# Performance work log

Measured on AMD Instinct MI355X. Metric: run time of the kernel, lower is better.

The kernel has to match this reference:

```python
import jax, jax.numpy as jnp
import numpy as np

# ---- config (matches init_kwargs) ----
C_IN, C_OUT = 128, 128
HYPER_OUT = 64            # hyper_out_size in DoubleConv
KB = C_IN // HYPER_OUT    # k = 2 blocks along input channels
HB = C_OUT // HYPER_OUT   # h = 2 blocks along output channels
Z_DIM, HID, SEIDEL_DIM = 128, 128, 48
R, F = 8, 3               # num_radii, filter size
BN_EPS = 1e-5


def _mlp_bank(z, W1, b1, W2, b2):
    # z: (S,); W1: (M,S,HID); returns (M, HID) embeddings from M distinct MLPs
    h = jax.nn.relu(jnp.einsum('s,msh->mh', z, W1) + b1)
    return jax.nn.relu(jnp.einsum('mh,mhg->mg', h, W2) + b2)


def _hyper(e, hw2, hb2, hw1, hb1):
    # Ha-style hypernetwork: e (Z_DIM,) -> kernel (64, 64, R, F, F)
    h_in = (e @ hw2 + hb2).reshape(HYPER_OUT, Z_DIM)
    h_fin = h_in @ hw1 + hb1  # (64, 64*R*F*F)
    return h_fin.reshape(HYPER_OUT, HYPER_OUT, R, F, F)


def _assemble(kernels, rows, cols):
    # kernels: (rows*cols, 64, 64, R, F, F) -> (rows*64, cols*64, R, F, F)
    k = kernels.reshape(rows, cols, HYPER_OUT, HYPER_OUT, R, F, F)
    k = k.transpose(0, 2, 1, 3, 4, 5, 6)
    return k.reshape(rows * HYPER_OUT, cols * HYPER_OUT, R, F, F)


def _interp_radii(w, Wdim):
    # trilinear interpolate (R,F,F)->(Wdim,F,F); F->F is identity, so linear along R
    # align_corners=False (PyTorch default)
    src = (jnp.arange(Wdim, dtype=jnp.float32) + 0.5) * (R / Wdim) - 0.5
    src = jnp.clip(src, 0.0, R - 1.0)
    i0 = jnp.floor(src).astype(jnp.int32)
    i1 = jnp.minimum(i0 + 1, R - 1)
    t = (src - i0.astype(jnp.float32))[None, None, :, None, None]
    return w[:, :, i0] * (1.0 - t) + w[:, :, i1] * t  # (co, ci, Wdim, F, F)


def _lri_conv(x, w):
    # x: (c_in, H, W); w: (c_out, c_in, R, F, F); padding=1, k=3
    c_in, H, W = x.shape
    xp = jnp.concatenate([x[:, -1:, :], x, x[:, :1, :]], axis=1)  # circular pad H
    xp = jnp.pad(xp, ((0, 0), (0, 0), (1, 1)))                    # zero pad W
    # patches laid out (c, di, dj) to match F.unfold
    pat = jnp.stack([xp[:, di:di + H, dj:dj + W]
                     for di in range(3) for dj in range(3)], axis=1)  # (c_in, 9, H, W)
    pat = pat.reshape(c_in * 9, H, W).transpose(1, 2, 0)              # (H, W, c_in*9)
    wi = _interp_radii(w, W)                                          # (co, ci, W, F, F)
    wu = wi.transpose(0, 2, 1, 3, 4).reshape(w.shape[0], W, c_in * 9) # (co, W, ci*9)
    return jnp.einsum('hwj,cwj->chw', pat, wu)                        # (co, H, W)


def _bn_eval(x, gamma, beta):
    # eval-mode BatchNorm2d with running_mean=0, running_var=1
    scale = gamma / jnp.sqrt(1.0 + BN_EPS)
    return x * scale[:, None, None] + beta[:, None, None]


def setup_inputs() -> dict:
    key = jax.random.key(0)
    ks = jax.random.split(key, 20)
    B, H, W = 2, 256, 128
    n1 = HB * KB   # 4 MLPs for first conv
    n2 = HB * HB   # 4 MLPs for second conv
    inp = {
        'x': jax.random.normal(ks[0], (B, C_IN, H, W), jnp.float32),
        'seidel': jax.random.normal(ks[1], (B, SEIDEL_DIM), jnp.float32),
        'm1_W1': jax.random.normal(ks[2], (n1, SEIDEL_DIM, HID)) * 0.1,
        'm1_b1': jnp.zeros((n1, HID)),
        'm1_W2': jax.random.normal(ks[3], (n1, HID, HID)) * 0.08,
        'm1_b2': jnp.zeros((n1, HID)),
        'm2_W1': jax.random.normal(ks[4], (n2, SEIDEL_DIM, HID)) * 0.1,
        'm2_b1': jnp.zeros((n2, HID)),
        'm2_W2': jax.random.normal(ks[5], (n2, HID, HID)) * 0.08,
        'm2_b2': jnp.zeros((n2, HID)),
        'hyp_w2': jax.random.normal(ks[6], (Z_DIM, HYPER_OUT * Z_DIM)) * 0.02,
        'hyp_b2': jnp.zeros((HYPER_OUT * Z_DIM,)),
        'hyp_w1': jax.random.normal(ks[7], (Z_DIM, HYPER_OUT * R * F * F)) * 0.02,
        'hyp_b1': jnp.zeros((HYPER_OUT * R * F * F,)),
        'bn1_g': jnp.ones((C_OUT,)), 'bn1_b': jnp.zeros((C_OUT,)),
        'bn2_g': jnp.ones((C_OUT,)), 'bn2_b': jnp.zeros((C_OUT,)),
    }
    return inp


def reference(x, seidel, m1_W1, m1_b1, m1_W2, m1_b2, m2_W1, m2_b1, m2_W2, m2_b2,
              hyp_w2, hyp_b2, hyp_w1, hyp_b1, bn1_g, bn1_b, bn2_g, bn2_b):
    hyper = lambda e: _hyper(e, hyp_w2, hyp_b2, hyp_w1, hyp_b1)

    def one_sample(x_i, z_i):
        emb1 = _mlp_bank(z_i, m1_W1, m1_b1, m1_W2, m1_b2)   # (h*k, Z)
        w1 = _assemble(jax.vmap(hyper)(emb1), HB, KB)        # (c_out, c_in, R, F, F)
        emb2 = _mlp_bank(z_i, m2_W1, m2_b1, m2_W2, m2_b2)   # (h*h, Z)
        w2 = _assemble(jax.vmap(hyper)(emb2), HB, HB)        # (c_out, c_out, R, F, F)
        y = jax.nn.relu(_bn_eval(_lri_conv(x_i, w1), bn1_g, bn1_b))
        y = jax.nn.relu(_bn_eval(_lri_conv(y, w2), bn2_g, bn2_b))
        return y

    return jax.vmap(one_sample)(x, seidel)  # (B, c_out, H, W)
```

## Files before the change

### kernel.cpp

```cpp
#include <hip/hip_runtime.h>
#include <hip/hip_bf16.h>

typedef _Float16 f16;
typedef _Float16 half8 __attribute__((ext_vector_type(8)));
typedef _Float16 half4_t __attribute__((ext_vector_type(4)));
typedef float floatx16 __attribute__((ext_vector_type(16)));

__device__ __forceinline__ void gll16(const void* g, void* l) {
    __builtin_amdgcn_global_load_lds(
        (const __attribute__((address_space(1))) void*)g,
        (__attribute__((address_space(3))) void*)l, 16, 0, 0);
}

__global__ __launch_bounds__(256) void embed_a(
    const float* __restrict__ seidel,
    const float* __restrict__ m1W1, const float* __restrict__ m1b1,
    const float* __restrict__ m1W2, const float* __restrict__ m1b2,
    const float* __restrict__ m2W1, const float* __restrict__ m2b1,
    const float* __restrict__ m2W2, const float* __restrict__ m2b2,
    float* __restrict__ eout)
{
    int combo = blockIdx.x;
    int s = combo >> 3, conv = (combo >> 2) & 1, m = combo & 3;
    const float* W1 = conv ? m2W1 : m1W1;
    const float* b1 = conv ? m2b1 : m1b1;
    const float* W2 = conv ? m2W2 : m1W2;
    const float* b2 = conv ? m2b2 : m1b2;
    __shared__ float zs[48], hbuf[128];
    int tid = threadIdx.x;
    if (tid < 48) zs[tid] = seidel[s*48 + tid];
    __syncthreads();
    if (tid < 128) {
        float a = b1[m*128 + tid];
        for (int i = 0; i < 48; ++i) a += zs[i] * W1[(m*48 + i)*128 + tid];
        hbuf[tid] = fmaxf(a, 0.f);
    }
    __syncthreads();
    if (tid < 128) {
        float a = b2[m*128 + tid];
        for (int i = 0; i < 128; ++i) a += hbuf[i] * W2[(m*128 + i)*128 + tid];
        eout[combo*128 + tid] = fmaxf(a, 0.f);
    }
}

__global__ __launch_bounds__(128) void embed_b3(
    const float* __restrict__ eout, const float* __restrict__ hw2,
    const float* __restrict__ hb2, float* __restrict__ hin)
{
    __shared__ float es[16][128];
    int tid = threadIdx.x;
    int j = blockIdx.x*128 + tid;
    for (int i = tid; i < 2048; i += 128) es[i >> 7][i & 127] = eout[i];
    __syncthreads();
    float acc[16];
    float b = hb2[j];
    #pragma unroll
    for (int c = 0; c < 16; ++c) acc[c] = b;
    for (int i = 0; i < 128; ++i) {
        float wv = hw2[(size_t)i*8192 + j];
        #pragma unroll
        for (int c = 0; c < 16; ++c) acc[c] += es[c][i]*wv;
    }
    #pragma unroll
    for (int c = 0; c < 16; ++c) hin[(size_t)c*8192 + j] = acc[c];
}

__global__ void hw1t_kernel(const float* __restrict__ in, float* __restrict__ out)
{
    __shared__ float tile[32][33];
    int j0 = blockIdx.x*32, k0 = blockIdx.y*32;
    int tx = threadIdx.x, ty = threadIdx.y;
    #pragma unroll
    for (int i = 0; i < 4; ++i) tile[ty + i*8][tx] = in[(size_t)(k0 + ty + i*8)*4608 + j0 + tx];
    __syncthreads();
    #pragma unroll
    for (int i = 0; i < 4; ++i) out[(size_t)(j0 + ty + i*8)*128 + k0 + tx] = tile[tx][ty + i*8];
}

__global__ __launch_bounds__(256) void hfin2_kernel(
    const float* __restrict__ hin, const float* __restrict__ hw1t,
    const float* __restrict__ hb1, f16* __restrict__ wtab)
{
    int c72 = blockIdx.x;
    int combo = blockIdx.y;
    int r = c72 / 9, tap = c72 - r*9;
    int s = combo >> 3, conv = (combo >> 2) & 1, m = combo & 3;
    __shared__ float hl[64][132];
    __shared__ float wt[64][132];
    __shared__ f16 ct[64][72];
    int tid = threadIdx.x;
    const float4* hsrc = (const float4*)(hin + (size_t)combo*8192);
    for (int i = tid; i < 2048; i += 256) {
        int a = i >> 5, kq = i & 31;
        *(float4*)&hl[a][kq*4] = hsrc[i];
    }
    for (int i = tid; i < 2048; i += 256) {
        int b = i >> 5, kq = i & 31;
        *(float4*)&wt[b][kq*4] = *(const float4*)(hw1t + (size_t)(b*72 + c72)*128 + kq*4);
    }
    __syncthreads();
    int ta = tid >> 4, tb = tid & 15;
    int a0 = ta*4, b0 = tb*4;
    float acc[4][4] = {};
    #pragma unroll 4
    for (int k4 = 0; k4 < 32; ++k4) {
        float4 A[4], B[4];
        #pragma unroll
        for (int i = 0; i < 4; ++i) A[i] = *(const float4*)&hl[a0 + i][k4*4];
        #pragma unroll
        for (int i = 0; i < 4; ++i) B[i] = *(const float4*)&wt[b0 + i][k4*4];
        #pragma unroll
        for (int i = 0; i < 4; ++i)
            #pragma unroll
            for (int j2 = 0; j2 < 4; ++j2)
                acc[i][j2] += A[i].x*B[j2].x + A[i].y*B[j2].y + A[i].z*B[j2].z + A[i].w*B[j2].w;
    }
    float bj[4];
    #pragma unroll
    for (int j2 = 0; j2 < 4; ++j2) bj[j2] = hb1[(b0 + j2)*72 + c72];
    #pragma unroll
    for (int i = 0; i < 4; ++i) {
        half4_t v;
        #pragma unroll
        for (int j2 = 0; j2 < 4; ++j2) v[j2] = (f16)(acc[i][j2] + bj[j2]);
        *(half4_t*)&ct[a0 + i][b0] = v;
    }
    __syncthreads();
    {
        int run = tid >> 1, hh = tid & 1;
        int a = run & 63, ch = run >> 6;
        int chunk = (m & 1)*2 + ch;
        int co = (m >> 1)*64 + a;
        size_t base = ((((size_t)(s*2 + conv)*8 + r)*4 + chunk)*9 + tap)*128 + co;
        f16* dst = wtab + base*32 + hh*16;
        const f16* src = &ct[a][ch*32 + hh*16];
        *(half8*)(dst)     = *(const half8*)(src);
        *(half8*)(dst + 8) = *(const half8*)(src + 8);
    }
}

__global__ __launch_bounds__(256) void xpose_cast2(
    const float* __restrict__ in, f16* __restrict__ out)
{
    __shared__ f16 tileT[128*136];
    int h = blockIdx.x, s = blockIdx.y;
    int tid = threadIdx.x;
    int cg = tid >> 5, q2 = tid & 31;
    const float* src = in + (size_t)s*4194304 + (size_t)h*128;
    for (int pass = 0; pass < 16; ++pass) {
        int c = pass*8 + cg;
        float4 v = *(const float4*)(src + (size_t)c*32768 + q2*4);
        tileT[(q2*4 + 0)*136 + c] = (f16)v.x;
        tileT[(q2*4 + 1)*136 + c] = (f16)v.y;
        tileT[(q2*4 + 2)*136 + c] = (f16)v.z;
        tileT[(q2*4 + 3)*136 + c] = (f16)v.w;
    }
    __syncthreads();
    int ww = tid >> 1, hf = tid & 1;
    const f16* srcT = &tileT[ww*136 + hf*64];
    f16* dst = out + (((size_t)(s*128 + ww)*256 + h)*128) + hf*64;
    #pragma unroll
    for (int i = 0; i < 8; ++i)
        *(float4*)(dst + i*8) = *(const float4*)(srcT + i*8);
}

__global__ void xpose_out(const float* __restrict__ in, float* __restrict__ out)
{
    __shared__ float tile[32][33];
    int sc = blockIdx.z;
    int w0 = blockIdx.x*32, h0 = blockIdx.y*32;
    int tx = threadIdx.x, ty = threadIdx.y;
    const float* src = in + ((size_t)sc*128 + w0)*256 + h0;
    #pragma unroll
    for (int i = 0; i < 4; ++i) tile[ty + i*8][tx] = src[(size_t)(ty + i*8)*256 + tx];
    __syncthreads();
    float* dst = out + ((size_t)sc*256 + h0)*128 + w0;
    #pragma unroll
    for (int i = 0; i < 4; ++i) dst[(size_t)(ty + i*8)*128 + tx] = tile[tx][ty + i*8];
}

template<int OUT_F16>
__global__ __launch_bounds__(512, 2) void conv_mfma7(
    const f16* __restrict__ xin,
    const f16* __restrict__ wtab,
    int conv,
    const float* __restrict__ bng, const float* __restrict__ bnb,
    void* __restrict__ outp)
{
    int flat = blockIdx.x;
    int xcd = flat & 7, idx = flat >> 3;
    int s = xcd >> 2;
    int w = (xcd & 3)*32 + idx;
    const f16* xs  = xin  + (size_t)s*4194304;
    const f16* wts = wtab + (size_t)(s*2 + conv)*1179648;

    float fsrc = fminf(fmaxf((w + 0.5f)*0.0625f - 0.5f, 0.f), 7.f);
    int r0 = (int)fsrc, r1 = min(r0 + 1, 7);
    f16 th = (f16)(fsrc - (float)r0);

    __shared__ __align__(16) char sbuf[123264];

    int tid = threadIdx.x;
    int lane = tid & 63, wid = tid >> 6;
    int wc = wid & 1, wh = wid >> 1;
    int l31 = lane & 31, lq = lane >> 5;

    if (w == 0 || w == 127) {
        int djo = (w == 0) ? 0 : 2;
        half8 z = {};
        for (int id = tid; id < 516; id += 512) {
            *(half8*)(sbuf + 73728 + (djo*516 + id)*16) = z;
            *(half8*)(sbuf + 73728 + 24768 + (djo*516 + id)*16) = z;
        }
    }
    __syncthreads();

    floatx16 acc[2][2];
    #pragma unroll
    for (int a = 0; a < 2; ++a)
        #pragma unroll
        for (int b = 0; b < 2; ++b) acc[a][b] = (floatx16)0.f;

    half8 wa[5], wb[5];

    auto stage_x = [&](int b, int hc) {
        char* xbase = sbuf + 73728 + b*24768;
        #pragma unroll
        for (int it = 0; it < 4; ++it) {
            int id = it*512 + tid;
            if (id < 1548) {
                int dj = id / 516;
                int rem = id - dj*516;
                int part = (rem >= 258) ? 1 : 0;
                int hp = rem - part*258;
                int wsg = w + dj - 1;
                if (wsg >= 0 && wsg < 128) {
                    const f16* src = xs + ((size_t)wsg*256 + ((hp - 1) & 255))*128
                                     + hc*16 + part*8;
                    char* ldst = xbase + (size_t)(it*512 + wid*64)*16;
                    gll16((const void*)src, (void*)ldst);
                }
            }
        }
    };
    auto load_w = [&](int hc) {
        int chunk = hc >> 1, half = hc & 1;
        #pragma unroll
        for (int p = 0; p < 5; ++p) {
            int sl = p*512 + tid;
            if (sl < 2304) {
                int tap = sl >> 8, rem = sl & 255;
                int part = rem >> 7, co = rem & 127;
                size_t off = (size_t)co*32 + half*16 + part*8;
                const f16* b0 = wts + (((size_t)(r0*4 + chunk)*9 + tap) << 12) + off;
                const f16* b1 = wts + (((size_t)(r1*4 + chunk)*9 + tap) << 12) + off;
                wa[p] = *(const half8*)b0;
                wb[p] = *(const half8*)b1;
            }
        }
    };
    auto write_w = [&](int b) {
        char* wbase = sbuf + b*36864;
        #pragma unroll
        for (int p = 0; p < 5; ++p) {
            int sl = p*512 + tid;
            if (sl < 2304) {
                half8 o = wa[p] + (wb[p] - wa[p])*th;
                *(half8*)(wbase + (size_t)sl*16) = o;
            }
        }
    };

    stage_x(0, 0);
    load_w(0);
    write_w(0);
    __syncthreads();

    for (int hc = 0; hc < 8; ++hc) {
        int cur = hc & 1;
        if (hc < 7) { stage_x(cur ^ 1, hc + 1); load_w(hc + 1); }
        const char* wb2 = sbuf + cur*36864;
        const char* xb  = sbuf + 73728 + cur*24768;
        __builtin_amdgcn_s_setprio(1);
        #pragma unroll
        for (int tap = 0; tap < 9; ++tap) {
            int di = tap/3, dj = tap - di*3;
            half8 af0 = *(const half8*)(wb2 + (size_t)((tap*2 + lq)*128 + wc*64 + l31)*16);
            half8 af1 = *(const half8*)(wb2 + (size_t)((tap*2 + lq)*128 + wc*64 + 32 + l31)*16);
            int hp = wh*64 + l31 + di;
            half8 bf0 = *(const half8*)(xb + (size_t)((dj*2 + lq)*258 + hp)*16);
            half8 bf1 = *(const half8*)(xb + (size_t)((dj*2 + lq)*258 + hp + 32)*16);
            acc[0][0] = __builtin_amdgcn_mfma_f32_32x32x16_f16(af0, bf0, acc[0][0], 0, 0, 0);
            acc[0][1] = __builtin_amdgcn_mfma_f32_32x32x16_f16(af0, bf1, acc[0][1], 0, 0, 0);
            acc[1][0] = __builtin_amdgcn_mfma_f32_32x32x16_f16(af1, bf0, acc[1][0], 0, 0, 0);
            acc[1][1] = __builtin_amdgcn_mfma_f32_32x32x16_f16(af1, bf1, acc[1][1], 0, 0, 0);
        }
        __builtin_amdgcn_s_setprio(0);
        if (hc < 7) write_w(cur ^ 1);
        __syncthreads();
    }

    float rs = rsqrtf(1.f + 1e-5f);
    if (OUT_F16) {
        f16* otile = (f16*)sbuf;
        f16* yout = (f16*)outp + ((size_t)(s*128 + w)*256)*128;
        #pragma unroll
        for (int ph = 0; ph < 2; ++ph) {
            __syncthreads();
            if ((wh >> 1) == ph) {
                #pragma unroll
                for (int ct = 0; ct < 2; ++ct) {
                    #pragma unroll
                    for (int ht = 0; ht < 2; ++ht) {
                        int hrow = (wh & 1)*64 + ht*32 + l31;
                        #pragma unroll
                        for (int rq = 0; rq < 4; ++rq) {
                            int cb = wc*64 + ct*32 + rq*8 + lq*4;
                            float4 g4 = *(const float4*)&bng[cb];
                            float4 b4 = *(const float4*)&bnb[cb];
                            half4_t v;
                            #pragma unroll
                            for (int e = 0; e < 4; ++e) {
                                float g = (&g4.x)[e], bb = (&b4.x)[e];
                                v[e] = (f16)fmaxf(acc[ct][ht][rq*4 + e]*g*rs + bb, 0.f);
                            }
                            *(half4_t*)&otile[hrow*136 + cb] = v;
                        }
                    }
                }
            }
            __syncthreads();
            {
                int hrow = tid >> 2, qc = tid & 3;
                const f16* srcT = &otile[hrow*136 + qc*32];
                f16* d = yout + (size_t)(ph*128 + hrow)*128 + qc*32;
                #pragma unroll
                for (int i = 0; i < 4; ++i)
                    *(float4*)(d + i*8) = *(const float4*)(srcT + i*8);
            }
        }
    } else {
        #pragma unroll
        for (int ct = 0; ct < 2; ++ct) {
            #pragma unroll
            for (int ht = 0; ht < 2; ++ht) {
                int hrow = wh*64 + ht*32 + l31;
                #pragma unroll
                for (int r = 0; r < 16; ++r) {
                    int co = wc*64 + ct*32 + (r & 3) + 8*(r >> 2) + 4*lq;
                    float v = fmaxf(acc[ct][ht][r]*bng[co]*rs + bnb[co], 0.f);
                    ((float*)outp)[((size_t)(s*128 + co)*128 + w)*256 + hrow] = v;
                }
            }
        }
    }
}

extern "C" void kernel_launch(void* const* d_in, const int* in_sizes, int n_in,
                              void* d_out, int out_size, void* d_ws, size_t ws_size,
                              hipStream_t stream) {
    const float* x      = (const float*)d_in[0];
    const float* seidel = (const float*)d_in[1];
    const float* m1W1 = (const float*)d_in[2];
    const float* m1b1 = (const float*)d_in[3];
    const float* m1W2 = (const float*)d_in[4];
    const float* m1b2 = (const float*)d_in[5];
    const float* m2W1 = (const float*)d_in[6];
    const float* m2b1 = (const float*)d_in[7];
    const float* m2W2 = (const float*)d_in[8];
    const float* m2b2 = (const float*)d_in[9];
    const float* hw2  = (const float*)d_in[10];
    const float* hb2  = (const float*)d_in[11];
    const float* hw1  = (const float*)d_in[12];
    const float* hb1  = (const float*)d_in[13];
    const float* bn1g = (const float*)d_in[14];
    const float* bn1b = (const float*)d_in[15];
    const float* bn2g = (const float*)d_in[16];
    const float* bn2b = (const float*)d_in[17];
    float* outp = (float*)d_out;

    char* wsb = (char*)d_ws;
    float* hin  = (float*)wsb;
    f16*   wtab = (f16*)(wsb + 524288);
    f16*   xt   = (f16*)(wsb + 9961472);
    f16*   y1t  = (f16*)(wsb + 26738688);
    float* y2t  = (float*)(wsb + 43515904);
    float* eout = (float*)xt;
    float* hw1t = y2t;

    embed_a<<<16, 256, 0, stream>>>(seidel, m1W1, m1b1, m1W2, m1b2,
                                    m2W1, m2b1, m2W2, m2b2, eout);
    embed_b3<<<64, 128, 0, stream>>>(eout, hw2, hb2, hin);
    hw1t_kernel<<<dim3(144, 4), dim3(32, 8), 0, stream>>>(hw1, hw1t);
    hfin2_kernel<<<dim3(72, 16), 256, 0, stream>>>(hin, hw1t, hb1, wtab);
    xpose_cast2<<<dim3(256, 2), 256, 0, stream>>>(x, xt);
    conv_mfma7<1><<<256, 512, 0, stream>>>(xt, wtab, 0, bn1g, bn1b, (void*)y1t);
    conv_mfma7<0><<<256, 512, 0, stream>>>(y1t, wtab, 1, bn2g, bn2b, (void*)y2t);
    xpose_out<<<dim3(4, 8, 256), dim3(32, 8), 0, stream>>>(y2t, outp);
}
```

Measured before the change: 160.1 us.

## Split conv blocks by output-channel half and relayout weight table for it

Each conv block now computes 64 output channels instead of 128, giving 512 blocks of 256 threads instead of 256 blocks of 512, with roughly half the shared memory. The weight table written by hfin2 is relaid out into 16-channel input chunks so each block reads its own channel half. The weight buffer is single-buffered in LDS and written after an extra barrier. The aim is more blocks per CU and a better split across XCDs. The cost is that each x tile is now loaded twice, once per channel-half block, and each iteration has an extra sync.

```diff
diff --git a/kernel.cpp b/kernel.cpp
--- a/kernel.cpp
+++ b/kernel.cpp
@@ -127,15 +127,12 @@
     }
     __syncthreads();
     {
-        int run = tid >> 1, hh = tid & 1;
-        int a = run & 63, ch = run >> 6;
-        int chunk = (m & 1)*2 + ch;
+        int a = tid & 63, q = tid >> 6;
+        int hc = (m & 1)*4 + q;
         int co = (m >> 1)*64 + a;
-        size_t base = ((((size_t)(s*2 + conv)*8 + r)*4 + chunk)*9 + tap)*128 + co;
-        f16* dst = wtab + base*32 + hh*16;
-        const f16* src = &ct[a][ch*32 + hh*16];
-        *(half8*)(dst)     = *(const half8*)(src);
-        *(half8*)(dst + 8) = *(const half8*)(src + 8);
+        f16* dst = wtab + (((((size_t)(s*2 + conv)*8 + r)*8 + hc)*9 + tap)*128 + co)*16;
+        *(half8*)(dst)     = *(const half8*)&ct[a][q*16];
+        *(half8*)(dst + 8) = *(const half8*)&ct[a][q*16 + 8];
     }
 }
 
@@ -180,17 +177,19 @@
 }
 
 template<int OUT_F16>
-__global__ __launch_bounds__(512, 2) void conv_mfma7(
+__global__ __launch_bounds__(256, 2) void conv_mfma9(
     const f16* __restrict__ xin,
     const f16* __restrict__ wtab,
     int conv,
     const float* __restrict__ bng, const float* __restrict__ bnb,
     void* __restrict__ outp)
 {
-    int flat = blockIdx.x;
-    int xcd = flat & 7, idx = flat >> 3;
-    int s = xcd >> 2;
-    int w = (xcd & 3)*32 + idx;
+    int b = blockIdx.x;
+    int xcd = b & 7, i = b >> 3;
+    int w = xcd*16 + (i & 15);
+    int cohalf = (i >> 4) & 1;
+    int s = i >> 5;
+    int co0 = cohalf << 6;
     const f16* xs  = xin  + (size_t)s*4194304;
     const f16* wts = wtab + (size_t)(s*2 + conv)*1179648;
 
@@ -198,96 +197,92 @@
     int r0 = (int)fsrc, r1 = min(r0 + 1, 7);
     f16 th = (f16)(fsrc - (float)r0);
 
-    __shared__ __align__(16) char sbuf[123264];
+    __shared__ __align__(16) char sbuf[67968];
 
     int tid = threadIdx.x;
     int lane = tid & 63, wid = tid >> 6;
-    int wc = wid & 1, wh = wid >> 1;
     int l31 = lane & 31, lq = lane >> 5;
 
     if (w == 0 || w == 127) {
         int djo = (w == 0) ? 0 : 2;
         half8 z = {};
-        for (int id = tid; id < 516; id += 512) {
-            *(half8*)(sbuf + 73728 + (djo*516 + id)*16) = z;
-            *(half8*)(sbuf + 73728 + 24768 + (djo*516 + id)*16) = z;
-        }
-    }
-    __syncthreads();
+        for (int id = tid; id < 516; id += 256) {
+            *(half8*)(sbuf + 18432 + (djo*516 + id)*16) = z;
+            *(half8*)(sbuf + 18432 + 24768 + (djo*516 + id)*16) = z;
+        }
+    }
 
     floatx16 acc[2][2];
     #pragma unroll
     for (int a = 0; a < 2; ++a)
         #pragma unroll
-        for (int b = 0; b < 2; ++b) acc[a][b] = (floatx16)0.f;
-
-    half8 wa[5], wb[5];
-
-    auto stage_x = [&](int b, int hc) {
-        char* xbase = sbuf + 73728 + b*24768;
-        #pragma unroll
-        for (int it = 0; it < 4; ++it) {
-            int id = it*512 + tid;
+        for (int c = 0; c < 2; ++c) acc[a][c] = (floatx16)0.f;
+
+    auto stage_x = [&](int bsel, int hc) {
+        char* xb = sbuf + 18432 + bsel*24768;
+        #pragma unroll
+        for (int it = 0; it < 7; ++it) {
+            int id = it*256 + tid;
             if (id < 1548) {
                 int dj = id / 516;
                 int rem = id - dj*516;
-                int part = (rem >= 258) ? 1 : 0;
+                int part = rem / 258;
                 int hp = rem - part*258;
                 int wsg = w + dj - 1;
                 if (wsg >= 0 && wsg < 128) {
                     const f16* src = xs + ((size_t)wsg*256 + ((hp - 1) & 255))*128
                                      + hc*16 + part*8;
-                    char* ldst = xbase + (size_t)(it*512 + wid*64)*16;
-                    gll16((const void*)src, (void*)ldst);
+                    gll16((const void*)src, (void*)(xb + (size_t)(it*256 + wid*64)*16));
                 }
             }
         }
     };
-    auto load_w = [&](int hc) {
-        int chunk = hc >> 1, half = hc & 1;
+
+    half8 lw[5] = {};
+    auto loadw = [&](int hc) {
         #pragma unroll
         for (int p = 0; p < 5; ++p) {
-            int sl = p*512 + tid;
-            if (sl < 2304) {
-                int tap = sl >> 8, rem = sl & 255;
-                int part = rem >> 7, co = rem & 127;
-                size_t off = (size_t)co*32 + half*16 + part*8;
-                const f16* b0 = wts + (((size_t)(r0*4 + chunk)*9 + tap) << 12) + off;
-                const f16* b1 = wts + (((size_t)(r1*4 + chunk)*9 + tap) << 12) + off;
-                wa[p] = *(const half8*)b0;
-                wb[p] = *(const half8*)b1;
-            }
+            int sl = p*256 + tid;
+            if (sl < 1152) {
+                int tap = sl >> 7, rem = sl & 127;
+                int col = rem >> 1, part = rem & 1;
+                size_t o0 = ((((size_t)r0*8 + hc)*9 + tap)*128 + co0 + col)*16 + part*8;
+                size_t o1 = ((((size_t)r1*8 + hc)*9 + tap)*128 + co0 + col)*16 + part*8;
+                half8 a = *(const half8*)(wts + o0);
+                half8 bb = *(const half8*)(wts + o1);
+                lw[p] = a + (bb - a)*th;
+            }
+            asm volatile("" : "+v"(lw[p]));
         }
     };
-    auto write_w = [&](int b) {
-        char* wbase = sbuf + b*36864;
+    auto write_w = [&]() {
         #pragma unroll
         for (int p = 0; p < 5; ++p) {
-            int sl = p*512 + tid;
-            if (sl < 2304) {
-                half8 o = wa[p] + (wb[p] - wa[p])*th;
-                *(half8*)(wbase + (size_t)sl*16) = o;
+            int sl = p*256 + tid;
+            if (sl < 1152) {
+                int tap = sl >> 7, rem = sl & 127;
+                int col = rem >> 1, part = rem & 1;
+                *(half8*)(sbuf + (size_t)((tap*2 + part)*64 + col)*16) = lw[p];
             }
         }
     };
 
     stage_x(0, 0);
-    load_w(0);
-    write_w(0);
+    loadw(0);
+    write_w();
     __syncthreads();
 
     for (int hc = 0; hc < 8; ++hc) {
         int cur = hc & 1;
-        if (hc < 7) { stage_x(cur ^ 1, hc + 1); load_w(hc + 1); }
-        const char* wb2 = sbuf + cur*36864;
-        const char* xb  = sbuf + 73728 + cur*24768;
+        if (hc < 7) { stage_x(cur ^ 1, hc + 1); loadw(hc + 1); }
+        const char* xb = sbuf + 18432 + cur*24768;
         __builtin_amdgcn_s_setprio(1);
         #pragma unroll
         for (int tap = 0; tap < 9; ++tap) {
             int di = tap/3, dj = tap - di*3;
-            half8 af0 = *(const half8*)(wb2 + (size_t)((tap*2 + lq)*128 + wc*64 + l31)*16);
-            half8 af1 = *(const half8*)(wb2 + (size_t)((tap*2 + lq)*128 + wc*64 + 32 + l31)*16);
-            int hp = wh*64 + l31 + di;
+            half8 af0 = *(const half8*)(sbuf + (size_t)((tap*2 + lq)*64 + l31)*16);
+            half8 af1 = *(const half8*)(sbuf + (size_t)((tap*2 + lq)*64 + 32 + l31)*16);
+            int hp = wid*64 + l31 + di;
             half8 bf0 = *(const half8*)(xb + (size_t)((dj*2 + lq)*258 + hp)*16);
             half8 bf1 = *(const half8*)(xb + (size_t)((dj*2 + lq)*258 + hp + 32)*16);
             acc[0][0] = __builtin_amdgcn_mfma_f32_32x32x16_f16(af0, bf0, acc[0][0], 0, 0, 0);
@@ -296,58 +291,50 @@
             acc[1][1] = __builtin_amdgcn_mfma_f32_32x32x16_f16(af1, bf1, acc[1][1], 0, 0, 0);
         }
         __builtin_amdgcn_s_setprio(0);
-        if (hc < 7) write_w(cur ^ 1);
         __syncthreads();
+        if (hc < 7) { write_w(); __syncthreads(); }
     }
 
     float rs = rsqrtf(1.f + 1e-5f);
     if (OUT_F16) {
         f16* otile = (f16*)sbuf;
-        f16* yout = (f16*)outp + ((size_t)(s*128 + w)*256)*128;
-        #pragma unroll
-        for (int ph = 0; ph < 2; ++ph) {
-            __syncthreads();
-            if ((wh >> 1) == ph) {
-                #pragma unroll
-                for (int ct = 0; ct < 2; ++ct) {
-                    #pragma unroll
-                    for (int ht = 0; ht < 2; ++ht) {
-                        int hrow = (wh & 1)*64 + ht*32 + l31;
-                        #pragma unroll
-                        for (int rq = 0; rq < 4; ++rq) {
-                            int cb = wc*64 + ct*32 + rq*8 + lq*4;
-                            float4 g4 = *(const float4*)&bng[cb];
-                            float4 b4 = *(const float4*)&bnb[cb];
-                            half4_t v;
-                            #pragma unroll
-                            for (int e = 0; e < 4; ++e) {
-                                float g = (&g4.x)[e], bb = (&b4.x)[e];
-                                v[e] = (f16)fmaxf(acc[ct][ht][rq*4 + e]*g*rs + bb, 0.f);
-                            }
-                            *(half4_t*)&otile[hrow*136 + cb] = v;
-                        }
-                    }
-                }
-            }
-            __syncthreads();
-            {
-                int hrow = tid >> 2, qc = tid & 3;
-                const f16* srcT = &otile[hrow*136 + qc*32];
-                f16* d = yout + (size_t)(ph*128 + hrow)*128 + qc*32;
-                #pragma unroll
-                for (int i = 0; i < 4; ++i)
-                    *(float4*)(d + i*8) = *(const float4*)(srcT + i*8);
-            }
-        }
-    } else {
         #pragma unroll
         for (int ct = 0; ct < 2; ++ct) {
             #pragma unroll
             for (int ht = 0; ht < 2; ++ht) {
-                int hrow = wh*64 + ht*32 + l31;
+                int hrow = wid*64 + ht*32 + l31;
+                #pragma unroll
+                for (int rq = 0; rq < 4; ++rq) {
+                    int cb = ct*32 + rq*8 + lq*4;
+                    float4 g4 = *(const float4*)&bng[co0 + cb];
+                    float4 b4 = *(const float4*)&bnb[co0 + cb];
+                    half4_t v;
+                    #pragma unroll
+                    for (int e = 0; e < 4; ++e) {
+                        float g = (&g4.x)[e], bb = (&b4.x)[e];
+                        v[e] = (f16)fmaxf(acc[ct][ht][rq*4 + e]*g*rs + bb, 0.f);
+                    }
+                    *(half4_t*)&otile[hrow*68 + cb] = v;
+                }
+            }
+        }
+        __syncthreads();
+        f16* yout = (f16*)outp + (size_t)(s*128 + w)*256*128 + co0;
+        #pragma unroll
+        for (int k = 0; k < 8; ++k) {
+            int id = k*256 + tid;
+            int h = id >> 3, q = id & 7;
+            *(float4*)(yout + (size_t)h*128 + q*8) = *(const float4*)&otile[h*68 + q*8];
+        }
+    } else {
+        #pragma unroll
+        for (int ct = 0; ct < 2; ++ct) {
+            #pragma unroll
+            for (int ht = 0; ht < 2; ++ht) {
+                int hrow = wid*64 + ht*32 + l31;
                 #pragma unroll
                 for (int r = 0; r < 16; ++r) {
-                    int co = wc*64 + ct*32 + (r & 3) + 8*(r >> 2) + 4*lq;
+                    int co = co0 + ct*32 + (r & 3) + 8*(r >> 2) + 4*lq;
                     float v = fmaxf(acc[ct][ht][r]*bng[co]*rs + bnb[co], 0.f);
                     ((float*)outp)[((size_t)(s*128 + co)*128 + w)*256 + hrow] = v;
                 }
@@ -394,7 +381,7 @@
     hw1t_kernel<<<dim3(144, 4), dim3(32, 8), 0, stream>>>(hw1, hw1t);
     hfin2_kernel<<<dim3(72, 16), 256, 0, stream>>>(hin, hw1t, hb1, wtab);
     xpose_cast2<<<dim3(256, 2), 256, 0, stream>>>(x, xt);
-    conv_mfma7<1><<<256, 512, 0, stream>>>(xt, wtab, 0, bn1g, bn1b, (void*)y1t);
-    conv_mfma7<0><<<256, 512, 0, stream>>>(y1t, wtab, 1, bn2g, bn2b, (void*)y2t);
+    conv_mfma9<1><<<512, 256, 0, stream>>>(xt, wtab, 0, bn1g, bn1b, (void*)y1t);
+    conv_mfma9<0><<<512, 256, 0, stream>>>(y1t, wtab, 1, bn2g, bn2b, (void*)y2t);
     xpose_out<<<dim3(4, 8, 256), dim3(32, 8), 0, stream>>>(y2t, outp);
 }
```

New measurement: 175.1 us. 1.09x slower.
